# Optimization experiments

Hardware: AMD Instinct MI355X
Metric: run time of the kernel (lower is better)

The kernel has to match this reference:

```python
import jax, jax.numpy as jnp
import numpy as np

D_MODEL = 1024
H = 16
D_K = D_MODEL // H


def setup_inputs() -> dict:
    key = jax.random.key(0)
    ks = jax.random.split(key, 9)
    s = 0.02
    x = jax.random.normal(ks[0], (2, 2048, D_MODEL), dtype=jnp.float32)
    Wq = jax.random.normal(ks[1], (D_MODEL, D_MODEL), dtype=jnp.float32) * s
    bq = jax.random.normal(ks[2], (D_MODEL,), dtype=jnp.float32) * s
    Wk = jax.random.normal(ks[3], (D_MODEL, D_MODEL), dtype=jnp.float32) * s
    bk = jax.random.normal(ks[4], (D_MODEL,), dtype=jnp.float32) * s
    Wv = jax.random.normal(ks[5], (D_MODEL, D_MODEL), dtype=jnp.float32) * s
    bv = jax.random.normal(ks[6], (D_MODEL,), dtype=jnp.float32) * s
    Wo = jax.random.normal(ks[7], (D_MODEL, D_MODEL), dtype=jnp.float32) * s
    bo = jax.random.normal(ks[8], (D_MODEL,), dtype=jnp.float32) * s
    return {"x": x, "Wq": Wq, "bq": bq, "Wk": Wk, "bk": bk,
            "Wv": Wv, "bv": bv, "Wo": Wo, "bo": bo}


def reference(x, Wq, bq, Wk, bk, Wv, bv, Wo, bo):
    b, s, _ = x.shape
    scale = 1.0 / jnp.sqrt(jnp.float32(D_K))
    # projections; [b, s, d] -> [b, h, s, d_k]
    def split_heads(t):
        return t.reshape(b, s, H, D_K).transpose(0, 2, 1, 3)
    q = split_heads(x @ Wq + bq)
    k = split_heads(x @ Wk + bk)
    v = split_heads(x @ Wv + bv)
    scores = jnp.einsum('bhqd,bhkd->bhqk', q, k) * scale  # [b,h,s,s]
    attn = jax.nn.softmax(scores, axis=-1)
    ctx = jnp.einsum('bhqk,bhkd->bhqd', attn, v)
    ctx = ctx.transpose(0, 2, 1, 3).reshape(b, s, D_MODEL)
    return ctx @ Wo + bo + x
```

## Files before the change

### kernel.cpp

```cpp
#include <hip/hip_runtime.h>
#include <hip/hip_bf16.h>
#include <stdint.h>

#define D_MODEL 1024
#define NH 16
#define DK 64
#define S_LEN 2048

typedef __attribute__((ext_vector_type(8))) __bf16 bf16x8;
typedef __attribute__((ext_vector_type(4))) float f32x4;

#define GLOBAL_AS __attribute__((address_space(1)))
#define LDS_AS    __attribute__((address_space(3)))

__device__ __forceinline__ void async16(const ushort* g, ushort* l) {
    __builtin_amdgcn_global_load_lds(
        (const GLOBAL_AS uint32_t*)(uintptr_t)(const void*)g,
        (LDS_AS uint32_t*)(uint32_t)(uintptr_t)(void*)l,
        16, 0, 0);
}

template <int N>
__device__ __forceinline__ void pipe_barrier() {
    asm volatile("s_waitcnt vmcnt(%0)\n\ts_barrier" :: "n"(N) : "memory");
}

__device__ __forceinline__ float fast_exp2(float x) {
    float r;
    asm("v_exp_f32 %0, %1" : "=v"(r) : "v"(x));
    return r;
}

__device__ __forceinline__ ushort f2bf(float f) {
    union { float f; uint32_t u; } v; v.f = f;
    uint32_t lsb = (v.u >> 16) & 1u;
    return (ushort)((v.u + 0x7fffu + lsb) >> 16);
}

__device__ __forceinline__ uint32_t packbf(float a, float b) {
    union { float f; uint32_t u; } x, y; x.f = a; y.f = b;
    return ((x.u + 0x8000u) >> 16) | ((y.u + 0x8000u) & 0xffff0000u);
}

__device__ __forceinline__ bf16x8 ldfrag(const ushort* p) {
    union { uint4 u; bf16x8 b; } cv;
    cv.u = *(const uint4*)p;
    return cv.b;
}


__global__ void cvt_x_kernel(const float* __restrict__ x, ushort* __restrict__ xb) {
    int i = blockIdx.x * 256 + threadIdx.x;
    float4 v = ((const float4*)x)[i];
    ushort4 o;
    o.x = f2bf(v.x); o.y = f2bf(v.y); o.z = f2bf(v.z); o.w = f2bf(v.w);
    ((ushort4*)xb)[i] = o;
}

__global__ void transpose_cvt4_kernel(
    const float* __restrict__ W0, const float* __restrict__ W1,
    const float* __restrict__ W2, const float* __restrict__ W3,
    ushort* __restrict__ D0, ushort* __restrict__ D1,
    ushort* __restrict__ D2, ushort* __restrict__ D3) {
    const float* W; ushort* D;
    switch (blockIdx.z) {
        case 0: W = W0; D = D0; break;
        case 1: W = W1; D = D1; break;
        case 2: W = W2; D = D2; break;
        default: W = W3; D = D3; break;
    }
    __shared__ float tile[32][33];
    int bx = blockIdx.x * 32, by = blockIdx.y * 32;
    int tx = threadIdx.x, ty = threadIdx.y;
#pragma unroll
    for (int j = 0; j < 32; j += 8)
        tile[ty + j][tx] = W[(size_t)(by + ty + j) * D_MODEL + bx + tx];
    __syncthreads();
#pragma unroll
    for (int j = 0; j < 32; j += 8)
        D[(size_t)(bx + ty + j) * D_MODEL + by + tx] = f2bf(tile[tx][ty + j]);
}

__global__ void cvt_bias_kernel(const float* __restrict__ bq, const float* __restrict__ bk,
                                const float* __restrict__ bv, float* __restrict__ out) {
    int i = blockIdx.x * 256 + threadIdx.x;
    float v = (i < 1024) ? bq[i] : (i < 2048 ? bk[i - 1024] : bv[i - 2048]);
    out[i] = v;
}

template <int MODE>
__global__ __launch_bounds__(256) void gemm_kernel(
    const ushort* __restrict__ A, const ushort* __restrict__ Bt,
    const float* __restrict__ bias,
    ushort* __restrict__ outQ, ushort* __restrict__ outK, ushort* __restrict__ outVt,
    const float* __restrict__ xres, float* __restrict__ outF) {
    constexpr int BN = (MODE == 0) ? 128 : 64;
    constexpr int NI = (MODE == 0) ? 4 : 2;
    constexpr int NS = (MODE == 0) ? 4 : 3;
    constexpr int ABUF = 4096;
    constexpr int BBUF = (MODE == 0) ? 4096 : 2048;
    constexpr int SMEM = (MODE == 0) ? 32768 : 24576;
    __shared__ __align__(16) ushort smem[SMEM];
    ushort* sAb = smem;
    ushort* sBb = smem + 4 * ABUF;

    const int tid = threadIdx.x;
    const int wave = tid >> 6, lane = tid & 63;
    const int lr = lane & 15, lq = lane >> 4;
    const int srow = lane >> 3, sp = lane & 7;

    const int bid = blockIdx.x;
    const int xcd = bid & 7, lb = bid >> 3;
    int bx, by;
    if (MODE == 0) { bx = xcd * 3 + (lb % 3); by = lb / 3; }
    else           { by = xcd * 4 + (lb & 3); bx = lb >> 2; }
    const int blockM = by * 128;
    const int blockN = bx * BN;
    const int waveM = (wave >> 1) * 64;
    const int waveN = (MODE == 0) ? (wave & 1) * 64 : (wave & 1) * 32;

    auto stage = [&](int k0, int buf) {
        ushort* a = sAb + buf * ABUF;
#pragma unroll
        for (int t = 0; t < 2; t++) {
            int Rb = wave * 16 + t * 8;
            int R = Rb + srow;
            int L = sp ^ (R & 7);
            int m = 2 * R + (L >> 2);
            int kc = L & 3;
            async16(&A[(size_t)(blockM + m) * D_MODEL + k0 + kc * 8], a + Rb * 64);
        }
        ushort* b = sBb + buf * BBUF;
        if (MODE == 0) {
#pragma unroll
            for (int t = 0; t < 2; t++) {
                int Rb = wave * 16 + t * 8;
                int R = Rb + srow;
                int L = sp ^ (R & 7);
                int n = 2 * R + (L >> 2);
                int kc = L & 3;
                async16(&Bt[(size_t)(blockN + n) * D_MODEL + k0 + kc * 8], b + Rb * 64);
            }
        } else {
            int Rb = wave * 8;
            int R = Rb + srow;
            int L = sp ^ (R & 7);
            int n = 2 * R + (L >> 2);
            int kc = L & 3;
            async16(&Bt[(size_t)(blockN + n) * D_MODEL + k0 + kc * 8], b + Rb * 64);
        }
    };

    const int RA = (waveM >> 1) + (lr >> 1);
    const int offA = RA * 64 + ((((lr & 1) * 4 + lq) ^ (RA & 7)) * 8);
    const int RB = (waveN >> 1) + (lr >> 1);
    const int offB = RB * 64 + ((((lr & 1) * 4 + lq) ^ (RB & 7)) * 8);

    f32x4 acc[4][NI] = {};

    stage(0, 0);
    stage(32, 1);
    stage(64, 2);
    pipe_barrier<2 * NS>();

#pragma unroll 4
    for (int k = 0; k < 32; k++) {
        const int buf = k & 3;
        if (k + 3 < 32) stage((k + 3) * 32, (k + 3) & 3);
        const ushort* a = sAb + buf * ABUF;
        const ushort* b = sBb + buf * BBUF;
        bf16x8 af[4], bfr[NI];
#pragma unroll
        for (int mi = 0; mi < 4; mi++)
            af[mi] = ldfrag(&a[offA + mi * 512]);
#pragma unroll
        for (int ni = 0; ni < NI; ni++)
            bfr[ni] = ldfrag(&b[offB + ni * 512]);
#pragma unroll
        for (int mi = 0; mi < 4; mi++)
#pragma unroll
            for (int ni = 0; ni < NI; ni++)
                acc[mi][ni] = __builtin_amdgcn_mfma_f32_16x16x32_bf16(
                    af[mi], bfr[ni], acc[mi][ni], 0, 0, 0);
        if (k < 30) pipe_barrier<2 * NS>();
        else if (k == 30) pipe_barrier<0>();
    }
    __syncthreads();

    const int bglob = blockM >> 11;
    const int sbase = blockM & 2047;

    if (MODE == 0) {
        const int which = bx >> 3;
        if (which < 2) {
            const float scale = (which == 0) ? 0.1803368801f : 1.0f;
#pragma unroll
            for (int ni = 0; ni < 4; ni++) {
                const int n_loc = waveN + ni * 16 + lr;
                const float bn = bias[blockN + n_loc];
#pragma unroll
                for (int mi = 0; mi < 4; mi++)
#pragma unroll
                    for (int r = 0; r < 4; r++) {
                        int m_loc = waveM + mi * 16 + lq * 4 + r;
                        smem[m_loc * 136 + n_loc] =
                            f2bf((acc[mi][ni][r] + bn) * scale);
                    }
            }
            __syncthreads();
            ushort* outp = (which == 0) ? outQ : outK;
            const int hbase = (which == 0) ? bx * 2 : (bx - 8) * 2;
#pragma unroll
            for (int j = 0; j < 8; j++) {
                int c = tid + j * 256;
                int m = c >> 4, nc = c & 15;
                int hh = nc >> 3, d8 = nc & 7;
                uint4 w = *(uint4*)&smem[m * 136 + nc * 8];
                size_t bh = (size_t)(bglob * NH + hbase + hh);
                *(uint4*)&outp[(bh * S_LEN + sbase + m) * DK + d8 * 8] = w;
            }
        } else {
#pragma unroll
            for (int ni = 0; ni < 4; ni++) {
                const int n_loc = waveN + ni * 16 + lr;
                const float bn = bias[blockN + n_loc];
#pragma unroll
                for (int mi = 0; mi < 4; mi++) {
                    uint2 w;
                    w.x = packbf(acc[mi][ni][0] + bn, acc[mi][ni][1] + bn);
                    w.y = packbf(acc[mi][ni][2] + bn, acc[mi][ni][3] + bn);
                    int m_base = waveM + mi * 16 + lq * 4;
                    *(uint2*)&smem[n_loc * 136 + m_base] = w;
                }
            }
            __syncthreads();
            const int hbase = (bx - 16) * 2;
#pragma unroll
            for (int j = 0; j < 8; j++) {
                int c = tid + j * 256;
                int n_loc = c >> 4, m8 = c & 15;
                int d = n_loc & 63, hh = n_loc >> 6;
                uint4 w = *(uint4*)&smem[n_loc * 136 + m8 * 8];
                size_t bh = (size_t)(bglob * NH + hbase + hh);
                *(uint4*)&outVt[(bh * DK + d) * S_LEN + sbase + m8 * 8] = w;
            }
        }
    } else {
        float* sCf = (float*)smem;
#pragma unroll
        for (int ni = 0; ni < 2; ni++) {
            const int n_loc = waveN + ni * 16 + lr;
            const float bn = bias[blockN + n_loc];
#pragma unroll
            for (int mi = 0; mi < 4; mi++)
#pragma unroll
                for (int r = 0; r < 4; r++) {
                    int m_loc = waveM + mi * 16 + lq * 4 + r;
                    sCf[m_loc * 68 + n_loc] = acc[mi][ni][r] + bn;
                }
        }
        __syncthreads();
#pragma unroll
        for (int j = 0; j < 8; j++) {
            int c = tid + j * 256;
            int m = c >> 4, nc = c & 15;
            float4 v = *(float4*)&sCf[m * 68 + nc * 4];
            size_t idx = (size_t)(blockM + m) * D_MODEL + blockN + nc * 4;
            float4 xr = *(const float4*)&xres[idx];
            v.x += xr.x; v.y += xr.y; v.z += xr.z; v.w += xr.w;
            *(float4*)&outF[idx] = v;
        }
    }
}

__global__ __launch_bounds__(256, 1) void attn_kernel(
    const ushort* __restrict__ Q, const ushort* __restrict__ Km,
    const ushort* __restrict__ Vt, ushort* __restrict__ ctx) {
    const int bid = blockIdx.x;
    const int xcd = bid & 7, lb = bid >> 3;
    const int bh = xcd * 4 + (lb & 3);
    const int qt = lb >> 2;
    const int q0 = qt * 256;
    __shared__ __align__(16) ushort sK[2][64 * 64];
    __shared__ __align__(16) ushort sV[2][64 * 64];
    __shared__ __align__(16) ushort sQP[4][64 * 64];
    const int tid = threadIdx.x;
    const int wave = tid >> 6, lane = tid & 63;
    const int lr = lane & 15, lq = lane >> 4;
    const int srow = lane >> 3, sp = lane & 7;
    const ushort* Qh = Q + (size_t)bh * S_LEN * DK;
    const ushort* Kh = Km + (size_t)bh * S_LEN * DK;
    const ushort* Vh = Vt + (size_t)bh * DK * S_LEN;
    ushort* sPw = sQP[wave];

#pragma unroll
    for (int t = 0; t < 8; t++) {
        int row = t * 8 + srow;
        int c = sp ^ (row & 7);
        async16(&Qh[(size_t)(q0 + wave * 64 + row) * DK + c * 8],
                &sPw[t * 8 * 64]);
    }

    auto stageKV = [&](int k0, int buf) {
#pragma unroll
        for (int t = 0; t < 2; t++) {
            int row = wave * 16 + t * 8 + srow;
            int c = sp ^ (row & 7);
            async16(&Kh[(size_t)(k0 + row) * DK + c * 8],
                    &sK[buf][(wave * 16 + t * 8) * 64]);
            async16(&Vh[(size_t)row * S_LEN + k0 + c * 8],
                    &sV[buf][(wave * 16 + t * 8) * 64]);
        }
    };

    stageKV(0, 0);
    __syncthreads();

    bf16x8 qf[4][2];
#pragma unroll
    for (int nj = 0; nj < 4; nj++)
#pragma unroll
        for (int kk = 0; kk < 2; kk++)
            qf[nj][kk] = ldfrag(&sPw[(nj * 16 + lr) * 64 +
                                     (((kk * 4 + lq) ^ (lr & 7)) * 8)]);

    f32x4 cacc[4][4] = {};
    float lsum[4] = {0.f, 0.f, 0.f, 0.f};

    for (int k = 0; k < 32; k++) {
        const int buf = k & 1;
        if (k + 1 < 32) stageKV((k + 1) * 64, buf ^ 1);
        const ushort* sk = sK[buf];
        const ushort* sv = sV[buf];

        f32x4 sacc[4][4] = {};
#pragma unroll
        for (int kk = 0; kk < 2; kk++) {
            bf16x8 kf[4];
            int swz = ((kk * 4 + lq) ^ (lr & 7)) * 8;
#pragma unroll
            for (int mi = 0; mi < 4; mi++)
                kf[mi] = ldfrag(&sk[(mi * 16 + lr) * 64 + swz]);
#pragma unroll
            for (int mi = 0; mi < 4; mi++)
#pragma unroll
                for (int nj = 0; nj < 4; nj++)
                    sacc[mi][nj] = __builtin_amdgcn_mfma_f32_16x16x32_bf16(
                        kf[mi], qf[nj][kk], sacc[mi][nj], 0, 0, 0);
        }

#pragma unroll
        for (int mi = 0; mi < 4; mi++)
#pragma unroll
            for (int nj = 0; nj < 4; nj++) {
                float p0 = fast_exp2(sacc[mi][nj][0]);
                float p1 = fast_exp2(sacc[mi][nj][1]);
                float p2 = fast_exp2(sacc[mi][nj][2]);
                float p3 = fast_exp2(sacc[mi][nj][3]);
                lsum[nj] += (p0 + p1) + (p2 + p3);
                uint2 w;
                w.x = packbf(p0, p1);
                w.y = packbf(p2, p3);
                int physc = (mi * 2 + (lq >> 1)) ^ (lr & 7);
                *(uint2*)&sPw[(nj * 16 + lr) * 64 + physc * 8 + (lq & 1) * 4] = w;
            }

#pragma unroll
        for (int ks = 0; ks < 2; ks++) {
            bf16x8 pf[4], vf[4];
            int swz = ((ks * 4 + lq) ^ (lr & 7)) * 8;
#pragma unroll
            for (int nj = 0; nj < 4; nj++)
                pf[nj] = ldfrag(&sPw[(nj * 16 + lr) * 64 + swz]);
#pragma unroll
            for (int nd = 0; nd < 4; nd++)
                vf[nd] = ldfrag(&sv[(nd * 16 + lr) * 64 + swz]);
#pragma unroll
            for (int nj = 0; nj < 4; nj++)
#pragma unroll
                for (int nd = 0; nd < 4; nd++)
                    cacc[nj][nd] = __builtin_amdgcn_mfma_f32_16x16x32_bf16(
                        pf[nj], vf[nd], cacc[nj][nd], 0, 0, 0);
        }

        if (k < 31) pipe_barrier<0>();
    }

    float inv[4];
#pragma unroll
    for (int nj = 0; nj < 4; nj++) {
        float l = lsum[nj];
        l += __shfl_xor(l, 16);
        l += __shfl_xor(l, 32);
        inv[nj] = __builtin_amdgcn_rcpf(l);
    }
    float invr[4][4];
#pragma unroll
    for (int nj = 0; nj < 4; nj++)
#pragma unroll
        for (int r = 0; r < 4; r++)
            invr[nj][r] = __shfl(inv[nj], lq * 4 + r);

    const int b = bh >> 4, h = bh & 15;
#pragma unroll
    for (int nj = 0; nj < 4; nj++)
#pragma unroll
        for (int nd = 0; nd < 4; nd++)
#pragma unroll
            for (int r = 0; r < 4; r++) {
                int qrow = q0 + wave * 64 + nj * 16 + lq * 4 + r;
                int d = nd * 16 + lr;
                float v = cacc[nj][nd][r] * invr[nj][r];
                ctx[(size_t)(b * S_LEN + qrow) * D_MODEL + h * DK + d] = f2bf(v);
            }
}


extern "C" void kernel_launch(void* const* d_in, const int* in_sizes, int n_in,
                              void* d_out, int out_size, void* d_ws, size_t ws_size,
                              hipStream_t stream) {
    const float* x  = (const float*)d_in[0];
    const float* Wq = (const float*)d_in[1];
    const float* bq = (const float*)d_in[2];
    const float* Wk = (const float*)d_in[3];
    const float* bk = (const float*)d_in[4];
    const float* Wv = (const float*)d_in[5];
    const float* bv = (const float*)d_in[6];
    const float* Wo = (const float*)d_in[7];
    const float* bo = (const float*)d_in[8];

    char* ws = (char*)d_ws;
    ushort* xb    = (ushort*)(ws);
    ushort* wqkv  = (ushort*)(ws + (8ull  << 20));
    ushort* wo_t  = (ushort*)(ws + (14ull << 20));
    ushort* qbuf  = (ushort*)(ws + (16ull << 20));
    ushort* kbuf  = (ushort*)(ws + (24ull << 20));
    ushort* vtb   = (ushort*)(ws + (32ull << 20));
    ushort* ctx   = (ushort*)(ws + (40ull << 20));
    float*  biasq = (float*)(ws + (48ull << 20));

    cvt_x_kernel<<<4096, 256, 0, stream>>>(x, xb);
    transpose_cvt4_kernel<<<dim3(32, 32, 4), dim3(32, 8), 0, stream>>>(
        Wq, Wk, Wv, Wo, wqkv, wqkv + 1024 * 1024, wqkv + 2 * 1024 * 1024, wo_t);
    cvt_bias_kernel<<<12, 256, 0, stream>>>(bq, bk, bv, biasq);

    gemm_kernel<0><<<768, 256, 0, stream>>>(
        xb, wqkv, biasq, qbuf, kbuf, vtb, nullptr, nullptr);
    attn_kernel<<<256, 256, 0, stream>>>(qbuf, kbuf, vtb, ctx);
    gemm_kernel<1><<<512, 256, 0, stream>>>(
        ctx, wo_t, bo, nullptr, nullptr, nullptr, x, (float*)d_out);
}
```

Before: 217.4 us.

## Split attention keys across waves with per-wave staging and cross-wave reduction

The attention kernel now processes 64 query rows per block, launched as 1024 blocks. Each of the four waves handles a disjoint 32-key slice of every 128-key tile and stages its own K and V data, so the per-iteration block barrier goes away. Partial context accumulators and row sums are then reduced across waves through shared memory, and the output is written as packed 16-byte stores. The aim is more blocks for occupancy (launch bounds raised to 2) and less synchronization, at the cost of an extra reduction epilogue and Q loaded per small block.

```diff
diff --git a/kernel.cpp b/kernel.cpp
--- a/kernel.cpp
+++ b/kernel.cpp
@@ -25,6 +25,11 @@
     asm volatile("s_waitcnt vmcnt(%0)\n\ts_barrier" :: "n"(N) : "memory");
 }
 
+template <int N>
+__device__ __forceinline__ void pipe_wait() {
+    asm volatile("s_waitcnt vmcnt(%0)" :: "n"(N) : "memory");
+}
+
 __device__ __forceinline__ float fast_exp2(float x) {
     float r;
     asm("v_exp_f32 %0, %1" : "=v"(r) : "v"(x));
@@ -45,6 +50,14 @@
 __device__ __forceinline__ bf16x8 ldfrag(const ushort* p) {
     union { uint4 u; bf16x8 b; } cv;
     cv.u = *(const uint4*)p;
+    return cv.b;
+}
+
+__device__ __forceinline__ bf16x8 ldfrag2(const ushort* p0, const ushort* p1) {
+    union { uint4 u; bf16x8 b; } cv;
+    uint2 a = *(const uint2*)p0;
+    uint2 b2 = *(const uint2*)p1;
+    cv.u = make_uint4(a.x, a.y, b2.x, b2.y);
     return cv.b;
 }
 
@@ -273,76 +286,87 @@
     }
 }
 
-__global__ __launch_bounds__(256, 1) void attn_kernel(
+__global__ __launch_bounds__(256, 2) void attn_kernel(
     const ushort* __restrict__ Q, const ushort* __restrict__ Km,
     const ushort* __restrict__ Vt, ushort* __restrict__ ctx) {
     const int bid = blockIdx.x;
     const int xcd = bid & 7, lb = bid >> 3;
     const int bh = xcd * 4 + (lb & 3);
     const int qt = lb >> 2;
-    const int q0 = qt * 256;
-    __shared__ __align__(16) ushort sK[2][64 * 64];
-    __shared__ __align__(16) ushort sV[2][64 * 64];
-    __shared__ __align__(16) ushort sQP[4][64 * 64];
+    const int q0 = qt * 64;
+    __shared__ __align__(16) ushort smem[32768];
     const int tid = threadIdx.x;
     const int wave = tid >> 6, lane = tid & 63;
     const int lr = lane & 15, lq = lane >> 4;
-    const int srow = lane >> 3, sp = lane & 7;
+    const int s8 = lane >> 3, p8 = lane & 7;
+    ushort* sKw = smem + wave * 4096;
+    ushort* sVw = smem + 16384 + wave * 2048;
+    ushort* sPw = smem + 24576 + wave * 2048;
     const ushort* Qh = Q + (size_t)bh * S_LEN * DK;
     const ushort* Kh = Km + (size_t)bh * S_LEN * DK;
     const ushort* Vh = Vt + (size_t)bh * DK * S_LEN;
-    ushort* sPw = sQP[wave];
-
-#pragma unroll
-    for (int t = 0; t < 8; t++) {
-        int row = t * 8 + srow;
-        int c = sp ^ (row & 7);
-        async16(&Qh[(size_t)(q0 + wave * 64 + row) * DK + c * 8],
-                &sPw[t * 8 * 64]);
-    }
-
-    auto stageKV = [&](int k0, int buf) {
-#pragma unroll
-        for (int t = 0; t < 2; t++) {
-            int row = wave * 16 + t * 8 + srow;
-            int c = sp ^ (row & 7);
-            async16(&Kh[(size_t)(k0 + row) * DK + c * 8],
-                    &sK[buf][(wave * 16 + t * 8) * 64]);
-            async16(&Vh[(size_t)row * S_LEN + k0 + c * 8],
-                    &sV[buf][(wave * 16 + t * 8) * 64]);
+    const int wsl = wave * 32;
+
+#pragma unroll
+    for (int t = 0; t < 2; t++) {
+        int row = wave * 16 + t * 8 + s8;
+        int c = p8 ^ (row & 7);
+        async16(&Qh[(size_t)(q0 + row) * DK + c * 8], &smem[(wave * 16 + t * 8) * 64]);
+    }
+    pipe_wait<0>();
+    __syncthreads();
+    bf16x8 qf[4][2];
+#pragma unroll
+    for (int nj = 0; nj < 4; nj++)
+#pragma unroll
+        for (int kk = 0; kk < 2; kk++)
+            qf[nj][kk] = ldfrag(&smem[(nj * 16 + lr) * 64 +
+                                      (((kk * 4 + lq) ^ (lr & 7)) * 8)]);
+    __syncthreads();
+
+    auto stageK = [&](int kt, int buf) {
+        ushort* dst = sKw + buf * 2048;
+#pragma unroll
+        for (int t = 0; t < 4; t++) {
+            int R = t * 8 + s8;
+            int c = p8 ^ (R & 7);
+            async16(&Kh[(size_t)(kt * 128 + wsl + R) * DK + c * 8], dst + t * 512);
         }
     };
-
-    stageKV(0, 0);
-    __syncthreads();
-
-    bf16x8 qf[4][2];
-#pragma unroll
-    for (int nj = 0; nj < 4; nj++)
-#pragma unroll
-        for (int kk = 0; kk < 2; kk++)
-            qf[nj][kk] = ldfrag(&sPw[(nj * 16 + lr) * 64 +
-                                     (((kk * 4 + lq) ^ (lr & 7)) * 8)]);
+    auto stageV = [&](int kt) {
+#pragma unroll
+        for (int t = 0; t < 4; t++) {
+            int R = t * 8 + s8;
+            int c = p8 ^ (R & 7);
+            int d = R * 2 + (c >> 2);
+            int kc = c & 3;
+            async16(&Vh[(size_t)d * S_LEN + kt * 128 + wsl + kc * 8], sVw + t * 512);
+        }
+    };
+
+    stageV(0);
+    stageK(0, 0);
+    stageK(1, 1);
+    pipe_wait<4>();
 
     f32x4 cacc[4][4] = {};
     float lsum[4] = {0.f, 0.f, 0.f, 0.f};
-
-    for (int k = 0; k < 32; k++) {
-        const int buf = k & 1;
-        if (k + 1 < 32) stageKV((k + 1) * 64, buf ^ 1);
-        const ushort* sk = sK[buf];
-        const ushort* sv = sV[buf];
-
-        f32x4 sacc[4][4] = {};
+    const int r7 = (lr >> 1) & 7;
+
+    for (int k = 0; k < 16; k++) {
+        const ushort* kb = sKw + (k & 1) * 2048;
+
+        f32x4 sacc[2][4] = {};
 #pragma unroll
         for (int kk = 0; kk < 2; kk++) {
-            bf16x8 kf[4];
-            int swz = ((kk * 4 + lq) ^ (lr & 7)) * 8;
-#pragma unroll
-            for (int mi = 0; mi < 4; mi++)
-                kf[mi] = ldfrag(&sk[(mi * 16 + lr) * 64 + swz]);
-#pragma unroll
-            for (int mi = 0; mi < 4; mi++)
+            bf16x8 kf[2];
+#pragma unroll
+            for (int mi = 0; mi < 2; mi++) {
+                int R = mi * 16 + lr;
+                kf[mi] = ldfrag(&kb[R * 64 + (((kk * 4 + lq) ^ (R & 7)) * 8)]);
+            }
+#pragma unroll
+            for (int mi = 0; mi < 2; mi++)
 #pragma unroll
                 for (int nj = 0; nj < 4; nj++)
                     sacc[mi][nj] = __builtin_amdgcn_mfma_f32_16x16x32_bf16(
@@ -350,7 +374,7 @@
         }
 
 #pragma unroll
-        for (int mi = 0; mi < 4; mi++)
+        for (int mi = 0; mi < 2; mi++)
 #pragma unroll
             for (int nj = 0; nj < 4; nj++) {
                 float p0 = fast_exp2(sacc[mi][nj][0]);
@@ -361,58 +385,107 @@
                 uint2 w;
                 w.x = packbf(p0, p1);
                 w.y = packbf(p2, p3);
-                int physc = (mi * 2 + (lq >> 1)) ^ (lr & 7);
-                *(uint2*)&sPw[(nj * 16 + lr) * 64 + physc * 8 + (lq & 1) * 4] = w;
-            }
-
-#pragma unroll
-        for (int ks = 0; ks < 2; ks++) {
-            bf16x8 pf[4], vf[4];
-            int swz = ((ks * 4 + lq) ^ (lr & 7)) * 8;
-#pragma unroll
-            for (int nj = 0; nj < 4; nj++)
-                pf[nj] = ldfrag(&sPw[(nj * 16 + lr) * 64 + swz]);
+                int R = nj * 8 + (lr >> 1);
+                int c = (lr & 1) * 8 + mi * 4 + lq;
+                *(uint2*)&sPw[R * 64 + ((c ^ r7) * 4)] = w;
+            }
+
+        bf16x8 pf[4], vf[4];
+#pragma unroll
+        for (int mq = 0; mq < 4; mq++) {
+            int R = mq * 8 + (lr >> 1);
+            int c0 = (lr & 1) * 8 + 2 * lq;
+            pf[mq] = ldfrag2(&sPw[R * 64 + ((c0 ^ r7) * 4)],
+                             &sPw[R * 64 + (((c0 + 1) ^ r7) * 4)]);
+        }
+#pragma unroll
+        for (int nd = 0; nd < 4; nd++) {
+            int d = nd * 16 + lr;
+            int R = nd * 8 + (lr >> 1);
+            int c = (lr & 1) * 4 + lq;
+            vf[nd] = ldfrag(&sVw[R * 64 + ((c ^ (R & 7)) * 8)]);
+        }
+#pragma unroll
+        for (int mq = 0; mq < 4; mq++)
 #pragma unroll
             for (int nd = 0; nd < 4; nd++)
-                vf[nd] = ldfrag(&sv[(nd * 16 + lr) * 64 + swz]);
-#pragma unroll
-            for (int nj = 0; nj < 4; nj++)
-#pragma unroll
-                for (int nd = 0; nd < 4; nd++)
-                    cacc[nj][nd] = __builtin_amdgcn_mfma_f32_16x16x32_bf16(
-                        pf[nj], vf[nd], cacc[nj][nd], 0, 0, 0);
-        }
-
-        if (k < 31) pipe_barrier<0>();
-    }
-
-    float inv[4];
+                cacc[mq][nd] = __builtin_amdgcn_mfma_f32_16x16x32_bf16(
+                    pf[mq], vf[nd], cacc[mq][nd], 0, 0, 0);
+
+        if (k < 14) {
+            stageV(k + 1);
+            stageK(k + 2, k & 1);
+            pipe_wait<4>();
+        } else if (k == 14) {
+            stageV(15);
+            pipe_wait<0>();
+        }
+    }
+
 #pragma unroll
     for (int nj = 0; nj < 4; nj++) {
         float l = lsum[nj];
         l += __shfl_xor(l, 16);
         l += __shfl_xor(l, 32);
-        inv[nj] = __builtin_amdgcn_rcpf(l);
-    }
-    float invr[4][4];
-#pragma unroll
-    for (int nj = 0; nj < 4; nj++)
-#pragma unroll
-        for (int r = 0; r < 4; r++)
-            invr[nj][r] = __shfl(inv[nj], lq * 4 + r);
-
-    const int b = bh >> 4, h = bh & 15;
-#pragma unroll
-    for (int nj = 0; nj < 4; nj++)
-#pragma unroll
-        for (int nd = 0; nd < 4; nd++)
-#pragma unroll
-            for (int r = 0; r < 4; r++) {
-                int qrow = q0 + wave * 64 + nj * 16 + lq * 4 + r;
-                int d = nd * 16 + lr;
-                float v = cacc[nj][nd][r] * invr[nj][r];
-                ctx[(size_t)(b * S_LEN + qrow) * D_MODEL + h * DK + d] = f2bf(v);
-            }
+        lsum[nj] = l;
+    }
+    float* red0 = (float*)smem;
+    float* red1 = (float*)(smem + 8192);
+    float* ls0  = (float*)(smem + 16384);
+    float* ls1  = (float*)(smem + 16512);
+    __syncthreads();
+    if (wave == 1 || wave == 3) {
+        float* rd = (wave == 1) ? red0 : red1;
+        float* ls = (wave == 1) ? ls0 : ls1;
+#pragma unroll
+        for (int mq = 0; mq < 4; mq++)
+#pragma unroll
+            for (int nd = 0; nd < 4; nd++)
+#pragma unroll
+                for (int r = 0; r < 4; r++)
+                    rd[(mq * 16 + lq * 4 + r) * 64 + nd * 16 + lr] = cacc[mq][nd][r];
+        if (lq == 0)
+#pragma unroll
+            for (int nj = 0; nj < 4; nj++) ls[nj * 16 + lr] = lsum[nj];
+    }
+    __syncthreads();
+    if (wave == 0 || wave == 2) {
+        float* rd = (wave == 0) ? red0 : red1;
+        float* ls = (wave == 0) ? ls0 : ls1;
+#pragma unroll
+        for (int mq = 0; mq < 4; mq++)
+#pragma unroll
+            for (int nd = 0; nd < 4; nd++)
+#pragma unroll
+                for (int r = 0; r < 4; r++)
+                    rd[(mq * 16 + lq * 4 + r) * 64 + nd * 16 + lr] += cacc[mq][nd][r];
+        if (lq == 0)
+#pragma unroll
+            for (int nj = 0; nj < 4; nj++) ls[nj * 16 + lr] += lsum[nj];
+    }
+    __syncthreads();
+
+    {
+        int q = tid >> 2, dg = (tid & 3) * 16;
+        float inv = __builtin_amdgcn_rcpf(ls0[q] + ls1[q]);
+        float s[16];
+#pragma unroll
+        for (int i = 0; i < 16; i += 4) {
+            f32x4 a = *(f32x4*)&red0[q * 64 + dg + i];
+            f32x4 b2 = *(f32x4*)&red1[q * 64 + dg + i];
+            s[i] = (a[0] + b2[0]) * inv; s[i + 1] = (a[1] + b2[1]) * inv;
+            s[i + 2] = (a[2] + b2[2]) * inv; s[i + 3] = (a[3] + b2[3]) * inv;
+        }
+        uint4 o0, o1;
+        o0.x = packbf(s[0], s[1]);  o0.y = packbf(s[2], s[3]);
+        o0.z = packbf(s[4], s[5]);  o0.w = packbf(s[6], s[7]);
+        o1.x = packbf(s[8], s[9]);  o1.y = packbf(s[10], s[11]);
+        o1.z = packbf(s[12], s[13]); o1.w = packbf(s[14], s[15]);
+        const int b = bh >> 4, h = bh & 15;
+        size_t base = (size_t)(b * S_LEN + q0 + q) * D_MODEL + h * DK + dg;
+        *(uint4*)&ctx[base] = o0;
+        *(uint4*)&ctx[base + 8] = o1;
+    }
 }
 
 
@@ -446,7 +519,7 @@
 
     gemm_kernel<0><<<768, 256, 0, stream>>>(
         xb, wqkv, biasq, qbuf, kbuf, vtb, nullptr, nullptr);
-    attn_kernel<<<256, 256, 0, stream>>>(qbuf, kbuf, vtb, ctx);
+    attn_kernel<<<1024, 256, 0, stream>>>(qbuf, kbuf, vtb, ctx);
     gemm_kernel<1><<<512, 256, 0, stream>>>(
         ctx, wo_t, bo, nullptr, nullptr, nullptr, x, (float*)d_out);
 }
```

Result: no change. 214.9 us (-1.1%).
